# Kernel tuning notes

Hardware: AMD Instinct MI355X
Metric: run time of the kernel (lower is better)

## Reference

```python
import jax, jax.numpy as jnp
import numpy as np
from jax import lax


def setup_inputs() -> dict:
    key = jax.random.key(0)
    ks = jax.random.split(key, 5)
    B, T, D, H = 128, 512, 256, 512
    s = 1.0 / np.sqrt(H)  # PyTorch LSTMCell init scale
    return {
        "x": jax.random.normal(ks[0], (B, T, D), dtype=jnp.float32),
        "W_ih": jax.random.uniform(ks[1], (4 * H, D), jnp.float32, -s, s),
        "W_hh": jax.random.uniform(ks[2], (4 * H, H), jnp.float32, -s, s),
        "b_ih": jax.random.uniform(ks[3], (4 * H,), jnp.float32, -s, s),
        "b_hh": jax.random.uniform(ks[4], (4 * H,), jnp.float32, -s, s),
    }


def reference(x, W_ih, W_hh, b_ih, b_hh):
    B, T, D = x.shape
    H = W_hh.shape[1]
    # Precompute input projections for all timesteps in one big GEMM: [B,T,4H]
    x_proj = jnp.einsum("btd,gd->btg", x, W_ih) + b_ih + b_hh

    def step(carry, xp_t):
        h, c = carry
        gates = xp_t + h @ W_hh.T  # [B, 4H]
        i, f, g, o = jnp.split(gates, 4, axis=-1)  # PyTorch gate order i,f,g,o
        c = jax.nn.sigmoid(f) * c + jax.nn.sigmoid(i) * jnp.tanh(g)
        h = jax.nn.sigmoid(o) * jnp.tanh(c)
        return (h, c), h

    h0 = jnp.zeros((B, H), x.dtype)
    (_, _), hs = lax.scan(step, (h0, h0), jnp.swapaxes(x_proj, 0, 1))
    # hs: [T, B, H] -> torch.cat(outputs, dim=0).unsqueeze(0) == [1, T*B, H]
    return hs.reshape(T * B, H)[None]
```

## Files before the change

### kernel.cpp

```cpp
#include <hip/hip_runtime.h>

#define B_ 128
#define T_ 512
#define D_ 256
#define H_ 512
#define GG_ 32
#define BG_ 8

typedef __bf16 bf16x8 __attribute__((ext_vector_type(8)));
typedef float  f32x4  __attribute__((ext_vector_type(4)));
typedef unsigned int u32;
typedef unsigned long long u64;
typedef u32    u32x4  __attribute__((ext_vector_type(4)));

__device__ __align__(16) u32 g_ht[(size_t)T_ * B_ * H_];
__device__ u32 g_rf[T_ * BG_ * GG_ * 4];

__global__ void clear_flags() {
    int i = blockIdx.x * 256 + threadIdx.x;
    if (i < T_ * BG_ * GG_ * 4) g_rf[i] = 0u;
}

__device__ inline float sigmoidf_(float v) { return 1.f / (1.f + __expf(-v)); }
__device__ inline float tanhf_(float v)    { return 1.f - 2.f / (__expf(2.f * v) + 1.f); }

__global__ __launch_bounds__(256, 1)
void lstm_persistent(const float* __restrict__ x,
                     const float* __restrict__ Wih,
                     const float* __restrict__ Whh,
                     const float* __restrict__ bih,
                     const float* __restrict__ bhh,
                     float* __restrict__ out,
                     u32* __restrict__ ws)
{
    const int tid  = threadIdx.x;
    const int wv   = tid >> 6;
    const int lane = tid & 63;
    const int bg   = blockIdx.x & (BG_ - 1);
    const int gg   = blockIdx.x >> 3;

    const int lm = lane & 15;
    const int lq = lane >> 4;

    __shared__ int s_mode;
    if (tid == 0) {
        const u32 xcc = __builtin_amdgcn_s_getreg((31 << 11) | 20);
        u32* L = ws + bg;
        u32* M = ws + 8 + bg;
        if (gg == 0)
            __hip_atomic_store(L, xcc + 1u, __ATOMIC_RELAXED, __HIP_MEMORY_SCOPE_AGENT);
        u32 lv;
        while ((lv = __hip_atomic_load(L, __ATOMIC_RELAXED, __HIP_MEMORY_SCOPE_AGENT)) == 0u)
            __builtin_amdgcn_s_sleep(2);
        __hip_atomic_fetch_add(M, (lv == xcc + 1u) ? 1u : 0x10000u,
                               __ATOMIC_RELAXED, __HIP_MEMORY_SCOPE_AGENT);
        u32 mv;
        while ((((mv = __hip_atomic_load(M, __ATOMIC_RELAXED, __HIP_MEMORY_SCOPE_AGENT))
                 & 0xffffu) + (mv >> 16)) < (u32)GG_)
            __builtin_amdgcn_s_sleep(2);
        s_mode = (mv == (u32)GG_);
    }
    __syncthreads();
    const bool local_mode = (s_mode != 0);

    bf16x8 wih_hi[2][4], wih_lo[2][4];
    bf16x8 whh_hi[4][4], whh_lo[4][4];

    for (int gt = 0; gt < 4; ++gt) {
        const int grow = gt * 512 + gg * 16 + lm;
#pragma unroll
        for (int kt = 0; kt < 2; ++kt) {
            const float* p = Wih + (size_t)grow * D_ + wv * 64 + kt * 32 + lq * 8;
            bf16x8 hi, lo;
#pragma unroll
            for (int e = 0; e < 8; ++e) {
                float v = p[e];
                __bf16 h1 = (__bf16)v;
                hi[e] = h1; lo[e] = (__bf16)(v - (float)h1);
            }
            wih_hi[kt][gt] = hi; wih_lo[kt][gt] = lo;
        }
#pragma unroll
        for (int kt = 0; kt < 4; ++kt) {
            const float* p = Whh + (size_t)grow * H_ + wv * 128 + kt * 32 + lq * 8;
            bf16x8 hi, lo;
#pragma unroll
            for (int e = 0; e < 8; ++e) {
                float v = p[e];
                __bf16 h1 = (__bf16)v;
                hi[e] = h1; lo[e] = (__bf16)(v - (float)h1);
            }
            whh_hi[kt][gt] = hi; whh_lo[kt][gt] = lo;
        }
    }

    const int pj = tid & 15;
    const int pb = tid >> 4;
    float bias[4];
#pragma unroll
    for (int tp = 0; tp < 4; ++tp) {
        const int r = tp * 512 + gg * 16 + pj;
        bias[tp] = bih[r] + bhh[r];
    }
    float c = 0.f;

    __shared__ __align__(16) float gp[2][4][64][17];

    const int   xrow   = bg * 16 + lm;
    const float* xbase = x + (size_t)xrow * T_ * D_ + wv * 64;
    const u32 hoff_r = (u32)(bg * 16 + lm) * H_ + wv * 128;
    const u32 hoff_w = (u32)(bg * 16 + pb) * H_ + gg * 16 + pj;

    f32x4 xr0[2], xr1[2], xn0[2], xn1[2];
#pragma unroll
    for (int kt = 0; kt < 2; ++kt) {
        const float* p = xbase + kt * 32 + lq * 8;
        xr0[kt] = *(const f32x4*)p;
        xr1[kt] = *(const f32x4*)(p + 4);
    }

    for (int t = 0; t < T_; ++t) {
        f32x4 acc[4];
#pragma unroll
        for (int gt = 0; gt < 4; ++gt) acc[gt] = (f32x4){0.f, 0.f, 0.f, 0.f};

#pragma unroll
        for (int kt = 0; kt < 2; ++kt) {
            bf16x8 ahi, alo;
#pragma unroll
            for (int e = 0; e < 4; ++e) {
                __bf16 h1 = (__bf16)xr0[kt][e];
                ahi[e] = h1; alo[e] = (__bf16)(xr0[kt][e] - (float)h1);
                __bf16 h2 = (__bf16)xr1[kt][e];
                ahi[e + 4] = h2; alo[e + 4] = (__bf16)(xr1[kt][e] - (float)h2);
            }
#pragma unroll
            for (int gt = 0; gt < 4; ++gt) {
                acc[gt] = __builtin_amdgcn_mfma_f32_16x16x32_bf16(ahi, wih_hi[kt][gt], acc[gt], 0, 0, 0);
                acc[gt] = __builtin_amdgcn_mfma_f32_16x16x32_bf16(ahi, wih_lo[kt][gt], acc[gt], 0, 0, 0);
                acc[gt] = __builtin_amdgcn_mfma_f32_16x16x32_bf16(alo, wih_hi[kt][gt], acc[gt], 0, 0, 0);
            }
        }

        if (t > 0) {
            const u32* fb = &g_rf[(u32)(t - 1) * (BG_ * GG_ * 4) + bg * (GG_ * 4) + 32 * wv];
            int spins = 0;
            while (true) {
                u32 v;
                if (spins < 256) {
                    v = __hip_atomic_load(fb + (lane & 31), __ATOMIC_RELAXED,
                                          __HIP_MEMORY_SCOPE_AGENT);
                } else {
                    v = __hip_atomic_fetch_add((u32*)fb + (lane & 31), 0u,
                                               __ATOMIC_RELAXED, __HIP_MEMORY_SCOPE_AGENT);
                }
                if (__all(v != 0u)) break;
                __builtin_amdgcn_s_sleep(1);
                ++spins;
            }
            __builtin_amdgcn_sched_barrier(0);

            const u32* hp = &g_ht[(size_t)(t - 1) * (B_ * H_) + hoff_r];
            u32 wd[4][8];
            if (local_mode) {
#pragma unroll
                for (int kt = 0; kt < 4; ++kt) {
                    u32x4 a = *(const u32x4*)(hp + kt * 32 + lq * 8);
                    u32x4 b = *(const u32x4*)(hp + kt * 32 + lq * 8 + 4);
#pragma unroll
                    for (int e = 0; e < 4; ++e) { wd[kt][e] = a[e]; wd[kt][e + 4] = b[e]; }
                }
            } else {
#pragma unroll
                for (int kt = 0; kt < 4; ++kt) {
                    const u64* q = (const u64*)(hp + kt * 32 + lq * 8);
#pragma unroll
                    for (int e = 0; e < 4; ++e) {
                        u64 v = __hip_atomic_load(q + e, __ATOMIC_RELAXED,
                                                  __HIP_MEMORY_SCOPE_AGENT);
                        wd[kt][2 * e] = (u32)v; wd[kt][2 * e + 1] = (u32)(v >> 32);
                    }
                }
            }

#pragma unroll
            for (int kt = 0; kt < 4; ++kt) {
                bf16x8 ahi, alo;
#pragma unroll
                for (int e = 0; e < 8; ++e) {
                    const u32 w = wd[kt][e];
                    ahi[e] = __builtin_bit_cast(__bf16, (unsigned short)(w & 0xffffu));
                    alo[e] = __builtin_bit_cast(__bf16, (unsigned short)(w >> 16));
                }
#pragma unroll
                for (int gt = 0; gt < 4; ++gt) {
                    acc[gt] = __builtin_amdgcn_mfma_f32_16x16x32_bf16(ahi, whh_hi[kt][gt], acc[gt], 0, 0, 0);
                    acc[gt] = __builtin_amdgcn_mfma_f32_16x16x32_bf16(ahi, whh_lo[kt][gt], acc[gt], 0, 0, 0);
                    acc[gt] = __builtin_amdgcn_mfma_f32_16x16x32_bf16(alo, whh_hi[kt][gt], acc[gt], 0, 0, 0);
                }
            }
        }

        __builtin_amdgcn_sched_barrier(0);
        if (t < T_ - 1) {
            const float* pn = xbase + (size_t)(t + 1) * D_;
#pragma unroll
            for (int kt = 0; kt < 2; ++kt) {
                const float* p = pn + kt * 32 + lq * 8;
                xn0[kt] = *(const f32x4*)p;
                xn1[kt] = *(const f32x4*)(p + 4);
            }
        }
        __builtin_amdgcn_sched_barrier(0);

        const int pbuf = t & 1;
#pragma unroll
        for (int gt = 0; gt < 4; ++gt)
            *(f32x4*)&gp[pbuf][wv][gt * 16 + lm][lq * 4] = acc[gt];
        __syncthreads();

        float gate[4];
#pragma unroll
        for (int tp = 0; tp < 4; ++tp) {
            const int g = tp * 16 + pj;
            gate[tp] = gp[pbuf][0][g][pb] + gp[pbuf][1][g][pb] +
                       gp[pbuf][2][g][pb] + gp[pbuf][3][g][pb] + bias[tp];
        }
        const float ig = sigmoidf_(gate[0]);
        const float fg = sigmoidf_(gate[1]);
        const float gv = tanhf_(gate[2]);
        const float og = sigmoidf_(gate[3]);
        c = fg * c + ig * gv;
        const float h = og * tanhf_(c);

        const __bf16 hh = (__bf16)h;
        const __bf16 hl = (__bf16)(h - (float)hh);
        const u32 packed = (u32)__builtin_bit_cast(unsigned short, hh) |
                           ((u32)__builtin_bit_cast(unsigned short, hl) << 16);
        u32* hw = &g_ht[(size_t)t * (B_ * H_) + hoff_w];
        if (local_mode) *hw = packed;
        else __hip_atomic_store(hw, packed, __ATOMIC_RELAXED, __HIP_MEMORY_SCOPE_AGENT);

        if (t < T_ - 1) {
            __builtin_amdgcn_sched_barrier(0);
            __builtin_amdgcn_s_waitcnt(0);
            __builtin_amdgcn_sched_barrier(0);
            if (lane == 0) {
                u32* f = &g_rf[(u32)t * (BG_ * GG_ * 4) + bg * (GG_ * 4) + gg * 4 + wv];
                if (local_mode) *f = 1u;
                else __hip_atomic_store(f, 1u, __ATOMIC_RELAXED, __HIP_MEMORY_SCOPE_AGENT);
            }
            __builtin_amdgcn_sched_barrier(0);
        }

        __builtin_nontemporal_store(h, &out[((size_t)t * B_ + bg * 16 + pb) * H_ + gg * 16 + pj]);

#pragma unroll
        for (int kt = 0; kt < 2; ++kt) { xr0[kt] = xn0[kt]; xr1[kt] = xn1[kt]; }
    }
}

extern "C" void kernel_launch(void* const* d_in, const int* in_sizes, int n_in,
                              void* d_out, int out_size, void* d_ws, size_t ws_size,
                              hipStream_t stream) {
    const float* x   = (const float*)d_in[0];
    const float* Wih = (const float*)d_in[1];
    const float* Whh = (const float*)d_in[2];
    const float* bih = (const float*)d_in[3];
    const float* bhh = (const float*)d_in[4];
    float* out = (float*)d_out;
    u32* ws = (u32*)d_ws;

    hipMemsetAsync(d_ws, 0, 4096, stream);
    hipLaunchKernelGGL(clear_flags, dim3((T_ * BG_ * GG_ * 4 + 255) / 256), dim3(256), 0, stream);
    hipLaunchKernelGGL(lstm_persistent, dim3(GG_ * BG_), dim3(256), 0, stream,
                       x, Wih, Whh, bih, bhh, out, ws);
}
```

Baseline: 1.635 ms.

## Replace per-step ready flags with sentinel-poisoned hidden state polling

Removes the separate ready-flag array and the XCC locality detection. The hidden-state buffer is pre-filled with a sentinel value, and consumers poll the h data itself until no sentinel remains. This takes out the waitcnt-then-flag-store round trip on the recurrent critical path and lets the h load be issued before the input-projection MFMAs. It also buffers output h for 16 steps in shared memory before writing, and adds a 128 MB poison pass over g_ht in exchange. The scheme depends on the sentinel pattern never appearing as a real packed bf16 pair; 0xFFFF is a NaN pattern in bf16, so real finite values should not produce it.

```diff
diff --git a/kernel.cpp b/kernel.cpp
--- a/kernel.cpp
+++ b/kernel.cpp
@@ -6,6 +6,7 @@
 #define H_ 512
 #define GG_ 32
 #define BG_ 8
+#define SENT 0xFFFFFFFFu
 
 typedef __bf16 bf16x8 __attribute__((ext_vector_type(8)));
 typedef float  f32x4  __attribute__((ext_vector_type(4)));
@@ -14,11 +15,12 @@
 typedef u32    u32x4  __attribute__((ext_vector_type(4)));
 
 __device__ __align__(16) u32 g_ht[(size_t)T_ * B_ * H_];
-__device__ u32 g_rf[T_ * BG_ * GG_ * 4];
-
-__global__ void clear_flags() {
-    int i = blockIdx.x * 256 + threadIdx.x;
-    if (i < T_ * BG_ * GG_ * 4) g_rf[i] = 0u;
+
+__global__ void poison_ht() {
+    const size_t n = (size_t)T_ * B_ * H_ / 4;
+    const u32x4 v = {SENT, SENT, SENT, SENT};
+    for (size_t i = (size_t)blockIdx.x * 256 + threadIdx.x; i < n; i += (size_t)gridDim.x * 256)
+        __builtin_nontemporal_store(v, (u32x4*)g_ht + i);
 }
 
 __device__ inline float sigmoidf_(float v) { return 1.f / (1.f + __expf(-v)); }
@@ -42,27 +44,6 @@
     const int lm = lane & 15;
     const int lq = lane >> 4;
 
-    __shared__ int s_mode;
-    if (tid == 0) {
-        const u32 xcc = __builtin_amdgcn_s_getreg((31 << 11) | 20);
-        u32* L = ws + bg;
-        u32* M = ws + 8 + bg;
-        if (gg == 0)
-            __hip_atomic_store(L, xcc + 1u, __ATOMIC_RELAXED, __HIP_MEMORY_SCOPE_AGENT);
-        u32 lv;
-        while ((lv = __hip_atomic_load(L, __ATOMIC_RELAXED, __HIP_MEMORY_SCOPE_AGENT)) == 0u)
-            __builtin_amdgcn_s_sleep(2);
-        __hip_atomic_fetch_add(M, (lv == xcc + 1u) ? 1u : 0x10000u,
-                               __ATOMIC_RELAXED, __HIP_MEMORY_SCOPE_AGENT);
-        u32 mv;
-        while ((((mv = __hip_atomic_load(M, __ATOMIC_RELAXED, __HIP_MEMORY_SCOPE_AGENT))
-                 & 0xffffu) + (mv >> 16)) < (u32)GG_)
-            __builtin_amdgcn_s_sleep(2);
-        s_mode = (mv == (u32)GG_);
-    }
-    __syncthreads();
-    const bool local_mode = (s_mode != 0);
-
     bf16x8 wih_hi[2][4], wih_lo[2][4];
     bf16x8 whh_hi[4][4], whh_lo[4][4];
 
@@ -105,11 +86,13 @@
     float c = 0.f;
 
     __shared__ __align__(16) float gp[2][4][64][17];
+    __shared__ float s_hout[16][256];
 
     const int   xrow   = bg * 16 + lm;
     const float* xbase = x + (size_t)xrow * T_ * D_ + wv * 64;
     const u32 hoff_r = (u32)(bg * 16 + lm) * H_ + wv * 128;
     const u32 hoff_w = (u32)(bg * 16 + pb) * H_ + gg * 16 + pj;
+    const size_t ooff = (size_t)(bg * 16 + pb) * H_ + gg * 16 + pj;
 
     f32x4 xr0[2], xr1[2], xn0[2], xn1[2];
 #pragma unroll
@@ -119,10 +102,23 @@
         xr1[kt] = *(const f32x4*)(p + 4);
     }
 
+#define LOAD_HD() do {                                                                   \
+        _Pragma("unroll") for (int kt = 0; kt < 4; ++kt)                                 \
+        _Pragma("unroll") for (int e = 0; e < 4; ++e) {                                  \
+            u64 v = __hip_atomic_load(qb + kt * 16 + e, __ATOMIC_RELAXED,                \
+                                      __HIP_MEMORY_SCOPE_AGENT);                         \
+            wd[kt][2 * e] = (u32)v; wd[kt][2 * e + 1] = (u32)(v >> 32);                  \
+        }                                                                                \
+    } while (0)
+
     for (int t = 0; t < T_; ++t) {
         f32x4 acc[4];
 #pragma unroll
         for (int gt = 0; gt < 4; ++gt) acc[gt] = (f32x4){0.f, 0.f, 0.f, 0.f};
+
+        u32 wd[4][8];
+        const u64* qb = (const u64*)(g_ht + (size_t)(t > 0 ? t - 1 : 0) * (B_ * H_) + hoff_r) + lq * 4;
+        if (t > 0) LOAD_HD();
 
 #pragma unroll
         for (int kt = 0; kt < 2; ++kt) {
@@ -143,45 +139,17 @@
         }
 
         if (t > 0) {
-            const u32* fb = &g_rf[(u32)(t - 1) * (BG_ * GG_ * 4) + bg * (GG_ * 4) + 32 * wv];
-            int spins = 0;
             while (true) {
-                u32 v;
-                if (spins < 256) {
-                    v = __hip_atomic_load(fb + (lane & 31), __ATOMIC_RELAXED,
-                                          __HIP_MEMORY_SCOPE_AGENT);
-                } else {
-                    v = __hip_atomic_fetch_add((u32*)fb + (lane & 31), 0u,
-                                               __ATOMIC_RELAXED, __HIP_MEMORY_SCOPE_AGENT);
-                }
-                if (__all(v != 0u)) break;
+                int ok = 1;
+#pragma unroll
+                for (int kt = 0; kt < 4; ++kt)
+#pragma unroll
+                    for (int e = 0; e < 8; ++e) ok &= (wd[kt][e] != SENT);
+                if (__all(ok)) break;
                 __builtin_amdgcn_s_sleep(1);
-                ++spins;
+                LOAD_HD();
             }
             __builtin_amdgcn_sched_barrier(0);
-
-            const u32* hp = &g_ht[(size_t)(t - 1) * (B_ * H_) + hoff_r];
-            u32 wd[4][8];
-            if (local_mode) {
-#pragma unroll
-                for (int kt = 0; kt < 4; ++kt) {
-                    u32x4 a = *(const u32x4*)(hp + kt * 32 + lq * 8);
-                    u32x4 b = *(const u32x4*)(hp + kt * 32 + lq * 8 + 4);
-#pragma unroll
-                    for (int e = 0; e < 4; ++e) { wd[kt][e] = a[e]; wd[kt][e + 4] = b[e]; }
-                }
-            } else {
-#pragma unroll
-                for (int kt = 0; kt < 4; ++kt) {
-                    const u64* q = (const u64*)(hp + kt * 32 + lq * 8);
-#pragma unroll
-                    for (int e = 0; e < 4; ++e) {
-                        u64 v = __hip_atomic_load(q + e, __ATOMIC_RELAXED,
-                                                  __HIP_MEMORY_SCOPE_AGENT);
-                        wd[kt][2 * e] = (u32)v; wd[kt][2 * e + 1] = (u32)(v >> 32);
-                    }
-                }
-            }
 
 #pragma unroll
             for (int kt = 0; kt < 4; ++kt) {
@@ -237,27 +205,21 @@
         const __bf16 hl = (__bf16)(h - (float)hh);
         const u32 packed = (u32)__builtin_bit_cast(unsigned short, hh) |
                            ((u32)__builtin_bit_cast(unsigned short, hl) << 16);
-        u32* hw = &g_ht[(size_t)t * (B_ * H_) + hoff_w];
-        if (local_mode) *hw = packed;
-        else __hip_atomic_store(hw, packed, __ATOMIC_RELAXED, __HIP_MEMORY_SCOPE_AGENT);
-
-        if (t < T_ - 1) {
-            __builtin_amdgcn_sched_barrier(0);
-            __builtin_amdgcn_s_waitcnt(0);
-            __builtin_amdgcn_sched_barrier(0);
-            if (lane == 0) {
-                u32* f = &g_rf[(u32)t * (BG_ * GG_ * 4) + bg * (GG_ * 4) + gg * 4 + wv];
-                if (local_mode) *f = 1u;
-                else __hip_atomic_store(f, 1u, __ATOMIC_RELAXED, __HIP_MEMORY_SCOPE_AGENT);
-            }
-            __builtin_amdgcn_sched_barrier(0);
-        }
-
-        __builtin_nontemporal_store(h, &out[((size_t)t * B_ + bg * 16 + pb) * H_ + gg * 16 + pj]);
+        __hip_atomic_store(&g_ht[(size_t)t * (B_ * H_) + hoff_w], packed,
+                           __ATOMIC_RELAXED, __HIP_MEMORY_SCOPE_AGENT);
+
+        s_hout[t & 15][tid] = h;
+        if ((t & 15) == 15) {
+            const int t0 = t - 15;
+#pragma unroll
+            for (int k = 0; k < 16; ++k)
+                __builtin_nontemporal_store(s_hout[k][tid], &out[(size_t)(t0 + k) * (B_ * H_) + ooff]);
+        }
 
 #pragma unroll
         for (int kt = 0; kt < 2; ++kt) { xr0[kt] = xn0[kt]; xr1[kt] = xn1[kt]; }
     }
+#undef LOAD_HD
 }
 
 extern "C" void kernel_launch(void* const* d_in, const int* in_sizes, int n_in,
@@ -271,8 +233,7 @@
     float* out = (float*)d_out;
     u32* ws = (u32*)d_ws;
 
-    hipMemsetAsync(d_ws, 0, 4096, stream);
-    hipLaunchKernelGGL(clear_flags, dim3((T_ * BG_ * GG_ * 4 + 255) / 256), dim3(256), 0, stream);
+    hipLaunchKernelGGL(poison_ht, dim3(2048), dim3(256), 0, stream);
     hipLaunchKernelGGL(lstm_persistent, dim3(GG_ * BG_), dim3(256), 0, stream,
                        x, Wih, Whh, bih, bhh, out, ws);
 }
```

New measurement: 3.281 ms. +100.7%, slower.
